# Optimization experiments

Measured on AMD Instinct MI355X. Metric: run time of the kernel, lower is better.

Reference implementation:

```python
import jax, jax.numpy as jnp
import numpy as np

N_VERTS = 778
N_JOINTS_CHAIN = 16  # wrist + 15 articulated joints
N_JOINTS_ALL = 21
PARENTS = np.array([0, 0, 1, 2, 0, 4, 5, 0, 7, 8, 0, 10, 11, 0, 13, 14])


def rodrigues(r):
    """Axis-angle [N,3] -> rotation matrices [N,3,3] (matches torch quat2mat path)."""
    angle = jnp.linalg.norm(r + 1e-8, axis=1, keepdims=True)  # [N,1]
    axis = r / angle
    c = jnp.cos(angle)[..., None]  # [N,1,1]
    s = jnp.sin(angle)[..., None]
    x, y, z = axis[:, 0], axis[:, 1], axis[:, 2]
    zero = jnp.zeros_like(x)
    K = jnp.stack([zero, -z, y,
                   z, zero, -x,
                   -y, x, zero], axis=1).reshape(-1, 3, 3)
    eye = jnp.eye(3, dtype=r.dtype)
    return eye + s * K + (1.0 - c) * jnp.matmul(K, K)


def make_A(R, t):
    """R [B,3,3], t [B,3] -> homogeneous [B,4,4]."""
    B = R.shape[0]
    top = jnp.concatenate([R, t[:, :, None]], axis=2)  # [B,3,4]
    bottom = jnp.broadcast_to(jnp.array([[[0., 0., 0., 1.]]], dtype=R.dtype), (B, 1, 4))
    return jnp.concatenate([top, bottom], axis=1)


def setup_inputs() -> dict:
    key = jax.random.key(0)
    ks = jax.random.split(key, 10)
    B = 8192
    w = jax.random.uniform(ks[9], (N_VERTS, 16), dtype=jnp.float32)
    w = w / jnp.sum(w, axis=1, keepdims=True)  # LBS weights rows sum to 1
    Jr = jax.random.uniform(ks[6], (N_VERTS, N_JOINTS_ALL), dtype=jnp.float32)
    Jr = Jr / jnp.sum(Jr, axis=0, keepdims=True)
    return {
        "beta": jax.random.normal(ks[0], (B, 10), dtype=jnp.float32) * 0.5,
        "theta": jax.random.normal(ks[1], (B, 10), dtype=jnp.float32) * 0.5,
        "wrist_euler": jax.random.normal(ks[2], (B, 3), dtype=jnp.float32) * 0.3,
        "v_template": jax.random.normal(ks[3], (N_VERTS, 3), dtype=jnp.float32) * 0.05,
        "shapedirs": jax.random.normal(ks[4], (10, N_VERTS * 3), dtype=jnp.float32) * 0.01,
        "posedirs": jax.random.normal(ks[5], (135, N_VERTS * 3), dtype=jnp.float32) * 0.01,
        "J_regressor": Jr,
        "hands_comp": jax.random.normal(ks[7], (10, 45), dtype=jnp.float32) * 0.5,
        "hands_mean": jax.random.normal(ks[8], (45,), dtype=jnp.float32) * 0.1,
        "weights": w,
    }


def reference(beta, theta, wrist_euler, v_template, shapedirs, posedirs,
              J_regressor, hands_comp, hands_mean, weights):
    B = beta.shape[0]
    # shape blendshapes
    v_shaped = jnp.matmul(beta, shapedirs).reshape(B, N_VERTS, 3) + v_template
    # joints from shaped template: [B,21,3]
    J = jnp.einsum('bvc,vj->bjc', v_shaped, J_regressor)
    # pca pose -> per-joint axis-angle -> rotation matrices
    euler_pose = jnp.matmul(theta, hands_comp) + hands_mean          # [B,45]
    Rs = rodrigues(euler_pose.reshape(-1, 3)).reshape(B, 15, 3, 3)
    global_rot = rodrigues(wrist_euler.reshape(-1, 3)).reshape(B, 1, 3, 3)
    # pose blendshapes: (Rs - I) flattened
    pose_feature = (Rs - jnp.eye(3, dtype=Rs.dtype)).reshape(B, 135)
    v_posed = v_shaped + jnp.matmul(pose_feature, posedirs).reshape(B, N_VERTS, 3)
    # kinematic chain (16 joints, fixed small loop)
    Rs_all = jnp.concatenate([global_rot, Rs], axis=1)  # [B,16,3,3]
    Jc = J[:, :N_JOINTS_CHAIN, :]
    results = [make_A(Rs_all[:, 0], Jc[:, 0])]
    for i in range(1, N_JOINTS_CHAIN):
        p = int(PARENTS[i])
        A_local = make_A(Rs_all[:, i], Jc[:, i] - Jc[:, p])
        results.append(jnp.matmul(results[p], A_local))
    G = jnp.stack(results, axis=1)  # [B,16,4,4]
    # subtract rest-pose joint locations: A = G - G @ [J;0] in last column
    Jh = jnp.concatenate([Jc, jnp.zeros((B, N_JOINTS_CHAIN, 1), Jc.dtype)], axis=2)
    GJ = jnp.einsum('bjpq,bjq->bjp', G, Jh)  # [B,16,4]
    A = G - jnp.concatenate([jnp.zeros((B, N_JOINTS_CHAIN, 4, 3), G.dtype), GJ[..., None]], axis=3)
    # linear blend skinning
    T = jnp.einsum('vj,bjpq->bvpq', weights, A)  # [B,778,4,4]
    v_posed_h = jnp.concatenate([v_posed, jnp.ones((B, N_VERTS, 1), v_posed.dtype)], axis=2)
    verts = jnp.einsum('bvpq,bvq->bvp', T, v_posed_h)[:, :, :3]
    joints = jnp.einsum('bvc,vj->bjc', verts, J_regressor)  # [B,21,3]
    return joints
```

## Files before the change

kernel.cpp:

```cpp
#include <hip/hip_runtime.h>
#include <math.h>

#define NV 778
#define KROW 2334
#define KTOT 146
#define NCOL 1008
#define NPART 16
#define DTLD 160
#define PEXLD 1032

__global__ __launch_bounds__(64) void kA_pre(const float* __restrict__ shapedirs,
                                             const float* __restrict__ posedirs,
                                             const float* __restrict__ v_template,
                                             const float* __restrict__ Jreg,
                                             const float* __restrict__ wgt,
                                             float* __restrict__ SJ, float* __restrict__ J0,
                                             float* __restrict__ Q,  float* __restrict__ W2,
                                             float* __restrict__ DT, int w2_blocks)
{
    const int bid = blockIdx.x;
    const int t = threadIdx.x;
    if (bid < 48) {
        const int j = bid / 3, c = bid % 3;
        float acc[11];
#pragma unroll
        for (int k = 0; k < 11; ++k) acc[k] = 0.f;
        for (int v = t; v < NV; v += 64) {
            const float jr = Jreg[v*21 + j];
            acc[10] += v_template[v*3 + c] * jr;
#pragma unroll
            for (int k = 0; k < 10; ++k)
                acc[k] += shapedirs[(size_t)k*KROW + v*3 + c] * jr;
        }
#pragma unroll
        for (int k = 0; k < 11; ++k) {
            float s = acc[k];
#pragma unroll
            for (int off = 32; off >= 1; off >>= 1) s += __shfl_down(s, off, 64);
            acc[k] = s;
        }
        if (t == 0) {
#pragma unroll
            for (int k = 0; k < 10; ++k) SJ[k*48 + j*3 + c] = acc[k];
            J0[j*3 + c] = acc[10];
        }
    } else if (bid < 384) {
        const int m = bid - 48, j = m >> 4, jj = m & 15;
        float s = 0.f;
        for (int v = t; v < NV; v += 64)
            s += Jreg[v*21 + j] * wgt[v*16 + jj];
#pragma unroll
        for (int off = 32; off >= 1; off >>= 1) s += __shfl_down(s, off, 64);
        if (t == 0) Q[m] = s;
    } else if (bid < 384 + w2_blocks) {
        const int gi = (bid - 384)*64 + t;
        if (gi < NV*336) {
            const int v = gi / 336, m = gi % 336;
            const int j = m >> 4, jj = m & 15;
            W2[gi] = Jreg[v*21 + j] * wgt[v*16 + jj];
        }
    } else {
        const int v = bid - 384 - w2_blocks;
#pragma unroll
        for (int kk = 0; kk < 3; ++kk) {
            const int k = t + kk*64;
            if (k < KTOT) {
                const float* drow = (k < 10)  ? shapedirs + (size_t)k*KROW
                                  : (k < 145) ? posedirs + (size_t)(k-10)*KROW
                                              : v_template;
                DT[((size_t)0*NV + v)*DTLD + k] = drow[3*v + 0];
                DT[((size_t)1*NV + v)*DTLD + k] = drow[3*v + 1];
                DT[((size_t)2*NV + v)*DTLD + k] = drow[3*v + 2];
            }
        }
    }
}

__global__ __launch_bounds__(192) void k_pre2(const float* __restrict__ DT,
                                              const float* __restrict__ W2,
                                              float* __restrict__ PKpart)
{
    const int bid = blockIdx.x;
    const int j = bid % 21;
    const int c = (bid / 21) % 3;
    const int s = bid / 63;
    const int k = threadIdx.x;
    if (k >= KTOT) return;
    float acc[16];
#pragma unroll
    for (int q = 0; q < 16; ++q) acc[q] = 0.f;
    const int v0 = s*49, v1 = min(NV, v0 + 49);
    const float* dt = DT + ((size_t)c*NV)*DTLD + k;
    for (int v = v0; v < v1; ++v) {
        const float d = dt[(size_t)v*DTLD];
        const float4* wq = (const float4*)(W2 + (size_t)v*336 + j*16);
        const float4 w0 = wq[0], w1 = wq[1], w2 = wq[2], w3 = wq[3];
        acc[0]  += d*w0.x; acc[1]  += d*w0.y; acc[2]  += d*w0.z; acc[3]  += d*w0.w;
        acc[4]  += d*w1.x; acc[5]  += d*w1.y; acc[6]  += d*w1.z; acc[7]  += d*w1.w;
        acc[8]  += d*w2.x; acc[9]  += d*w2.y; acc[10] += d*w2.z; acc[11] += d*w2.w;
        acc[12] += d*w3.x; acc[13] += d*w3.y; acc[14] += d*w3.z; acc[15] += d*w3.w;
    }
    float* o = PKpart + ((size_t)s*KTOT + k)*NCOL + j*48 + c;
#pragma unroll
    for (int q = 0; q < 16; ++q) o[q*3] = acc[q];
}

__global__ void k_p3(const float4* __restrict__ PKpart, float4* __restrict__ PK)
{
    const int n4 = KTOT*NCOL/4;
    const int idx = blockIdx.x*256 + threadIdx.x;
    if (idx < n4) {
        float4 s = PKpart[idx];
#pragma unroll
        for (int p = 1; p < NPART; ++p) {
            const float4 v = PKpart[(size_t)p*n4 + idx];
            s.x += v.x; s.y += v.y; s.z += v.z; s.w += v.w;
        }
        PK[idx] = s;
    }
}

__global__ __launch_bounds__(256) void k2_pose(const float* __restrict__ beta,
                                               const float* __restrict__ theta,
                                               const float* __restrict__ wrist,
                                               const float* __restrict__ hc,
                                               const float* __restrict__ hm,
                                               const float* __restrict__ SJ,
                                               const float* __restrict__ J0,
                                               float* __restrict__ coefT,
                                               float* __restrict__ A_g, int B)
{
    __shared__ float Rs[16*144];
    __shared__ float cls[16*148];
    const int t = threadIdx.x;
    const int bl = t >> 4, i = t & 15;
    const int b = blockIdx.x*16 + bl;

    float r0, r1, r2;
    if (i == 0) {
        r0 = wrist[b*3+0]; r1 = wrist[b*3+1]; r2 = wrist[b*3+2];
#pragma unroll
        for (int k = 0; k < 10; ++k) cls[bl*148 + k] = beta[b*10 + k];
        cls[bl*148 + 145] = 1.0f;
    } else {
        const int col = (i-1)*3;
        float e0 = hm[col], e1 = hm[col+1], e2 = hm[col+2];
#pragma unroll
        for (int k = 0; k < 10; ++k) {
            const float th = theta[b*10 + k];
            e0 += th * hc[k*45 + col];
            e1 += th * hc[k*45 + col+1];
            e2 += th * hc[k*45 + col+2];
        }
        r0 = e0; r1 = e1; r2 = e2;
    }
    const float x_ = r0 + 1e-8f, y_ = r1 + 1e-8f, z_ = r2 + 1e-8f;
    const float angle = sqrtf(x_*x_ + y_*y_ + z_*z_);
    const float inv = 1.0f / angle;
    const float x = r0*inv, y = r1*inv, z = r2*inv;
    const float sn = sinf(angle), cs = cosf(angle);
    const float t1 = 1.0f - cs;
    float R[9];
    R[0] = 1.f - t1*(y*y + z*z);
    R[1] = -sn*z + t1*x*y;
    R[2] =  sn*y + t1*x*z;
    R[3] =  sn*z + t1*x*y;
    R[4] = 1.f - t1*(x*x + z*z);
    R[5] = -sn*x + t1*y*z;
    R[6] = -sn*y + t1*x*z;
    R[7] =  sn*x + t1*y*z;
    R[8] = 1.f - t1*(x*x + y*y);
#pragma unroll
    for (int q = 0; q < 9; ++q) Rs[bl*144 + i*9 + q] = R[q];
    if (i > 0) {
#pragma unroll
        for (int q = 0; q < 9; ++q)
            cls[bl*148 + 10 + (i-1)*9 + q] = R[q] - ((q==0||q==4||q==8) ? 1.f : 0.f);
    }
    __syncthreads();

    if (t < KTOT) {
        float tmp[16];
#pragma unroll
        for (int m = 0; m < 16; ++m) tmp[m] = cls[m*148 + t];
        float4* dst = (float4*)(coefT + (size_t)t*B + blockIdx.x*16);
        dst[0] = make_float4(tmp[0],  tmp[1],  tmp[2],  tmp[3]);
        dst[1] = make_float4(tmp[4],  tmp[5],  tmp[6],  tmp[7]);
        dst[2] = make_float4(tmp[8],  tmp[9],  tmp[10], tmp[11]);
        dst[3] = make_float4(tmp[12], tmp[13], tmp[14], tmp[15]);
    }

    if (t < 16) {
        const int b2 = blockIdx.x*16 + t;
        float bt[10];
#pragma unroll
        for (int k = 0; k < 10; ++k) bt[k] = beta[b2*10 + k];
        const float* Rb = Rs + t*144;
        float4* Ab = (float4*)(A_g + (size_t)b2*192);

        auto jointJ = [&](int j, float* o) {
            float j0 = J0[j*3+0], j1 = J0[j*3+1], j2 = J0[j*3+2];
#pragma unroll
            for (int k = 0; k < 10; ++k) {
                j0 += bt[k] * SJ[k*48 + j*3 + 0];
                j1 += bt[k] * SJ[k*48 + j*3 + 1];
                j2 += bt[k] * SJ[k*48 + j*3 + 2];
            }
            o[0] = j0; o[1] = j1; o[2] = j2;
        };

        float G0R[9], J0v[3];
#pragma unroll
        for (int q = 0; q < 9; ++q) G0R[q] = Rb[q];
        jointJ(0, J0v);
#pragma unroll
        for (int r = 0; r < 3; ++r) {
            const float at = J0v[r] - (G0R[r*3+0]*J0v[0] + G0R[r*3+1]*J0v[1] + G0R[r*3+2]*J0v[2]);
            Ab[r] = make_float4(G0R[r*3+0], G0R[r*3+1], G0R[r*3+2], at);
        }
        for (int ch = 0; ch < 5; ++ch) {
            float GpR[9], Gpt[3], Jp[3];
#pragma unroll
            for (int q = 0; q < 9; ++q) GpR[q] = G0R[q];
            Gpt[0]=J0v[0]; Gpt[1]=J0v[1]; Gpt[2]=J0v[2];
            Jp[0]=J0v[0];  Jp[1]=J0v[1];  Jp[2]=J0v[2];
            for (int s = 0; s < 3; ++s) {
                const int j = ch*3 + 1 + s;
                float Rl[9];
                const float* Rj = Rb + j*9;
#pragma unroll
                for (int q = 0; q < 9; ++q) Rl[q] = Rj[q];
                float Jc[3];
                jointJ(j, Jc);
                const float tl0 = Jc[0]-Jp[0], tl1 = Jc[1]-Jp[1], tl2 = Jc[2]-Jp[2];
                float GR[9], Gt[3];
#pragma unroll
                for (int r = 0; r < 3; ++r) {
#pragma unroll
                    for (int cc = 0; cc < 3; ++cc)
                        GR[r*3+cc] = GpR[r*3+0]*Rl[0*3+cc] + GpR[r*3+1]*Rl[1*3+cc] + GpR[r*3+2]*Rl[2*3+cc];
                    Gt[r] = GpR[r*3+0]*tl0 + GpR[r*3+1]*tl1 + GpR[r*3+2]*tl2 + Gpt[r];
                }
#pragma unroll
                for (int r = 0; r < 3; ++r) {
                    const float at = Gt[r] - (GR[r*3+0]*Jc[0] + GR[r*3+1]*Jc[1] + GR[r*3+2]*Jc[2]);
                    Ab[j*3 + r] = make_float4(GR[r*3+0], GR[r*3+1], GR[r*3+2], at);
                }
#pragma unroll
                for (int q = 0; q < 9; ++q) GpR[q] = GR[q];
                Gpt[0]=Gt[0]; Gpt[1]=Gt[1]; Gpt[2]=Gt[2];
                Jp[0]=Jc[0];  Jp[1]=Jc[1];  Jp[2]=Jc[2];
            }
        }
    }
}

__global__ __launch_bounds__(512) void k3_gemm(const float* __restrict__ coefT,
                                               const float* __restrict__ PK,
                                               const float* __restrict__ A_g,
                                               const float* __restrict__ Q,
                                               float* __restrict__ out, int B)
{
    __shared__ float Pex[8*PEXLD];
    const int t  = threadIdx.x;
    const int b0 = blockIdx.x * 16;
    const int l  = t;

    float acc[2][16];
#pragma unroll
    for (int e = 0; e < 16; ++e) { acc[0][e] = 0.f; acc[1][e] = 0.f; }

    if (l < 504) {
        const float* pkp = PK + 2*l;
        const float* cof = coefT + b0;
#pragma unroll 2
        for (int k = 0; k < KTOT; ++k) {
            const float2 p2 = *(const float2*)(pkp + (size_t)k*NCOL);
            const float4* cp = (const float4*)(cof + (size_t)k*B);
            const float4 c0 = cp[0], c1 = cp[1], c2 = cp[2], c3 = cp[3];
            const float cv[16] = {c0.x,c0.y,c0.z,c0.w, c1.x,c1.y,c1.z,c1.w,
                                  c2.x,c2.y,c2.z,c2.w, c3.x,c3.y,c3.z,c3.w};
#pragma unroll
            for (int e = 0; e < 16; ++e) {
                acc[0][e] += p2.x * cv[e];
                acc[1][e] += p2.y * cv[e];
            }
        }
    }

#pragma unroll
    for (int r = 0; r < 2; ++r) {
        __syncthreads();
        if (l < 504) {
            const int j  = (2*l) / 48;
            const int sc = j*49 + (2*l - 48*j);
#pragma unroll
            for (int bb = 0; bb < 8; ++bb)
                *(float2*)(&Pex[bb*PEXLD + sc]) =
                    make_float2(acc[0][r*8 + bb], acc[1][r*8 + bb]);
        }
        __syncthreads();
        if (t < 504) {
            const int bl = t / 63;
            const int rm = t % 63;
            const int j  = rm / 3, p = rm % 3;
            const int b  = b0 + r*8 + bl;
            const float4* Ab = ((const float4*)A_g) + (size_t)b*48;
            const float* Pr = Pex + bl*PEXLD + j*49;
            float s = 0.f;
#pragma unroll
            for (int jj = 0; jj < 16; ++jj) {
                const float4 a = Ab[jj*3 + p];
                s += a.x*Pr[jj*3+0] + a.y*Pr[jj*3+1] + a.z*Pr[jj*3+2]
                   + a.w*Q[j*16+jj];
            }
            out[(size_t)b0*63 + r*504 + t] = s;
        }
    }
}

extern "C" void kernel_launch(void* const* d_in, const int* in_sizes, int n_in,
                              void* d_out, int out_size, void* d_ws, size_t ws_size,
                              hipStream_t stream) {
    (void)n_in; (void)out_size; (void)ws_size;
    const float* beta       = (const float*)d_in[0];
    const float* theta      = (const float*)d_in[1];
    const float* wrist      = (const float*)d_in[2];
    const float* v_template = (const float*)d_in[3];
    const float* shapedirs  = (const float*)d_in[4];
    const float* posedirs   = (const float*)d_in[5];
    const float* Jreg       = (const float*)d_in[6];
    const float* hc         = (const float*)d_in[7];
    const float* hm         = (const float*)d_in[8];
    const float* wgt        = (const float*)d_in[9];
    float* out = (float*)d_out;
    const int B = in_sizes[0] / 10;

    float* ws = (float*)d_ws;
    size_t off = 0;
    auto alloc = [&](size_t n) { float* p = ws + off; off = (off + n + 63) & ~(size_t)63; return p; };
    float* SJ     = alloc(480);
    float* J0     = alloc(48);
    float* Q      = alloc(336);
    float* W2     = alloc((size_t)NV*336);
    float* DT     = alloc((size_t)3*NV*DTLD);
    float* PKpart = alloc((size_t)NPART*KTOT*NCOL);
    float* PK     = alloc((size_t)KTOT*NCOL);
    float* coefT  = alloc((size_t)KTOT*B);
    float* A_g    = alloc((size_t)B*192);

    const int w2_blocks = (NV*336 + 63)/64;
    kA_pre<<<384 + w2_blocks + NV, 64, 0, stream>>>(shapedirs, posedirs, v_template,
                                                    Jreg, wgt, SJ, J0, Q, W2, DT, w2_blocks);
    k2_pose<<<(B + 15)/16, 256, 0, stream>>>(beta, theta, wrist, hc, hm, SJ, J0, coefT, A_g, B);
    k_pre2<<<21*3*NPART, 192, 0, stream>>>(DT, W2, PKpart);
    k_p3<<<(KTOT*NCOL/4 + 255)/256, 256, 0, stream>>>((const float4*)PKpart, (float4*)PK);
    k3_gemm<<<dim3(B/16), 512, 0, stream>>>(coefT, PK, A_g, Q, out, B);
}
```

Before: 164.2 us.

## Merge precompute kernels and replace partial-sum reduction with atomics

The parameter precompute stages are cut from four launches to two. The PK partial-product kernel now runs inside the same launch as the pose kernel and adds its results straight into PK with atomicAdd, so the PKpart buffer and its separate reduction kernel are gone. The first kernel zeroes PK and moves to 256-thread blocks, with one wave per reduction row. Vertex splitting doubles to 32 parts so there are more parallel blocks, at the cost of many more float atomics and a summation order that is no longer deterministic.

```diff
diff --git a/kernel.cpp b/kernel.cpp
--- a/kernel.cpp
+++ b/kernel.cpp
@@ -5,27 +5,36 @@
 #define KROW 2334
 #define KTOT 146
 #define NCOL 1008
-#define NPART 16
+#define NPART 32
 #define DTLD 160
 #define PEXLD 1032
 
-__global__ __launch_bounds__(64) void kA_pre(const float* __restrict__ shapedirs,
-                                             const float* __restrict__ posedirs,
-                                             const float* __restrict__ v_template,
-                                             const float* __restrict__ Jreg,
-                                             const float* __restrict__ wgt,
-                                             float* __restrict__ SJ, float* __restrict__ J0,
-                                             float* __restrict__ Q,  float* __restrict__ W2,
-                                             float* __restrict__ DT, int w2_blocks)
+#define NB_RED 12
+#define NB_Q   84
+#define NB_W2  ((NV*336 + 255)/256)
+#define NB_DT  NV
+#define NB_Z   ((KTOT*NCOL + 255)/256)
+
+__global__ __launch_bounds__(256) void kA_all(const float* __restrict__ shapedirs,
+                                              const float* __restrict__ posedirs,
+                                              const float* __restrict__ v_template,
+                                              const float* __restrict__ Jreg,
+                                              const float* __restrict__ wgt,
+                                              float* __restrict__ SJ, float* __restrict__ J0,
+                                              float* __restrict__ Q,  float* __restrict__ W2,
+                                              float* __restrict__ DT, float* __restrict__ PK)
 {
     const int bid = blockIdx.x;
     const int t = threadIdx.x;
-    if (bid < 48) {
-        const int j = bid / 3, c = bid % 3;
+    const int wv = t >> 6, lane = t & 63;
+
+    if (bid < NB_RED) {
+        const int m = bid*4 + wv;
+        const int j = m / 3, c = m % 3;
         float acc[11];
 #pragma unroll
         for (int k = 0; k < 11; ++k) acc[k] = 0.f;
-        for (int v = t; v < NV; v += 64) {
+        for (int v = lane; v < NV; v += 64) {
             const float jr = Jreg[v*21 + j];
             acc[10] += v_template[v*3 + c] * jr;
 #pragma unroll
@@ -39,102 +48,91 @@
             for (int off = 32; off >= 1; off >>= 1) s += __shfl_down(s, off, 64);
             acc[k] = s;
         }
-        if (t == 0) {
+        if (lane == 0) {
 #pragma unroll
             for (int k = 0; k < 10; ++k) SJ[k*48 + j*3 + c] = acc[k];
             J0[j*3 + c] = acc[10];
         }
-    } else if (bid < 384) {
-        const int m = bid - 48, j = m >> 4, jj = m & 15;
+    } else if (bid < NB_RED + NB_Q) {
+        const int m = (bid - NB_RED)*4 + wv;
+        const int j = m >> 4, jj = m & 15;
         float s = 0.f;
-        for (int v = t; v < NV; v += 64)
+        for (int v = lane; v < NV; v += 64)
             s += Jreg[v*21 + j] * wgt[v*16 + jj];
 #pragma unroll
         for (int off = 32; off >= 1; off >>= 1) s += __shfl_down(s, off, 64);
-        if (t == 0) Q[m] = s;
-    } else if (bid < 384 + w2_blocks) {
-        const int gi = (bid - 384)*64 + t;
+        if (lane == 0) Q[m] = s;
+    } else if (bid < NB_RED + NB_Q + NB_W2) {
+        const int gi = (bid - NB_RED - NB_Q)*256 + t;
         if (gi < NV*336) {
             const int v = gi / 336, m = gi % 336;
             const int j = m >> 4, jj = m & 15;
             W2[gi] = Jreg[v*21 + j] * wgt[v*16 + jj];
         }
+    } else if (bid < NB_RED + NB_Q + NB_W2 + NB_DT) {
+        const int v = bid - NB_RED - NB_Q - NB_W2;
+        const int k = t;
+        if (k < KTOT) {
+            const float* drow = (k < 10)  ? shapedirs + (size_t)k*KROW
+                              : (k < 145) ? posedirs + (size_t)(k-10)*KROW
+                                          : v_template;
+            DT[((size_t)0*NV + v)*DTLD + k] = drow[3*v + 0];
+            DT[((size_t)1*NV + v)*DTLD + k] = drow[3*v + 1];
+            DT[((size_t)2*NV + v)*DTLD + k] = drow[3*v + 2];
+        }
     } else {
-        const int v = bid - 384 - w2_blocks;
-#pragma unroll
-        for (int kk = 0; kk < 3; ++kk) {
-            const int k = t + kk*64;
-            if (k < KTOT) {
-                const float* drow = (k < 10)  ? shapedirs + (size_t)k*KROW
-                                  : (k < 145) ? posedirs + (size_t)(k-10)*KROW
-                                              : v_template;
-                DT[((size_t)0*NV + v)*DTLD + k] = drow[3*v + 0];
-                DT[((size_t)1*NV + v)*DTLD + k] = drow[3*v + 1];
-                DT[((size_t)2*NV + v)*DTLD + k] = drow[3*v + 2];
-            }
-        }
+        const int idx = (bid - NB_RED - NB_Q - NB_W2 - NB_DT)*256 + t;
+        if (idx < KTOT*NCOL) PK[idx] = 0.f;
     }
 }
 
-__global__ __launch_bounds__(192) void k_pre2(const float* __restrict__ DT,
-                                              const float* __restrict__ W2,
-                                              float* __restrict__ PKpart)
-{
-    const int bid = blockIdx.x;
-    const int j = bid % 21;
-    const int c = (bid / 21) % 3;
-    const int s = bid / 63;
-    const int k = threadIdx.x;
-    if (k >= KTOT) return;
-    float acc[16];
-#pragma unroll
-    for (int q = 0; q < 16; ++q) acc[q] = 0.f;
-    const int v0 = s*49, v1 = min(NV, v0 + 49);
-    const float* dt = DT + ((size_t)c*NV)*DTLD + k;
-    for (int v = v0; v < v1; ++v) {
-        const float d = dt[(size_t)v*DTLD];
-        const float4* wq = (const float4*)(W2 + (size_t)v*336 + j*16);
-        const float4 w0 = wq[0], w1 = wq[1], w2 = wq[2], w3 = wq[3];
-        acc[0]  += d*w0.x; acc[1]  += d*w0.y; acc[2]  += d*w0.z; acc[3]  += d*w0.w;
-        acc[4]  += d*w1.x; acc[5]  += d*w1.y; acc[6]  += d*w1.z; acc[7]  += d*w1.w;
-        acc[8]  += d*w2.x; acc[9]  += d*w2.y; acc[10] += d*w2.z; acc[11] += d*w2.w;
-        acc[12] += d*w3.x; acc[13] += d*w3.y; acc[14] += d*w3.z; acc[15] += d*w3.w;
-    }
-    float* o = PKpart + ((size_t)s*KTOT + k)*NCOL + j*48 + c;
-#pragma unroll
-    for (int q = 0; q < 16; ++q) o[q*3] = acc[q];
-}
-
-__global__ void k_p3(const float4* __restrict__ PKpart, float4* __restrict__ PK)
-{
-    const int n4 = KTOT*NCOL/4;
-    const int idx = blockIdx.x*256 + threadIdx.x;
-    if (idx < n4) {
-        float4 s = PKpart[idx];
-#pragma unroll
-        for (int p = 1; p < NPART; ++p) {
-            const float4 v = PKpart[(size_t)p*n4 + idx];
-            s.x += v.x; s.y += v.y; s.z += v.z; s.w += v.w;
-        }
-        PK[idx] = s;
-    }
-}
-
-__global__ __launch_bounds__(256) void k2_pose(const float* __restrict__ beta,
-                                               const float* __restrict__ theta,
-                                               const float* __restrict__ wrist,
-                                               const float* __restrict__ hc,
-                                               const float* __restrict__ hm,
-                                               const float* __restrict__ SJ,
-                                               const float* __restrict__ J0,
-                                               float* __restrict__ coefT,
-                                               float* __restrict__ A_g, int B)
+__global__ __launch_bounds__(256) void k_mid(const float* __restrict__ DT,
+                                             const float* __restrict__ W2,
+                                             float* __restrict__ PK,
+                                             const float* __restrict__ beta,
+                                             const float* __restrict__ theta,
+                                             const float* __restrict__ wrist,
+                                             const float* __restrict__ hc,
+                                             const float* __restrict__ hm,
+                                             const float* __restrict__ SJ,
+                                             const float* __restrict__ J0,
+                                             float* __restrict__ coefT,
+                                             float* __restrict__ A_g, int B)
 {
     __shared__ float Rs[16*144];
     __shared__ float cls[16*148];
+    const int bid = blockIdx.x;
     const int t = threadIdx.x;
+
+    if (bid < 21*3*NPART) {
+        const int j = bid % 21;
+        const int c = (bid / 21) % 3;
+        const int s = bid / 63;
+        const int k = t;
+        if (k >= KTOT) return;
+        float acc[16];
+#pragma unroll
+        for (int q = 0; q < 16; ++q) acc[q] = 0.f;
+        const int v0 = s*25, v1 = min(NV, v0 + 25);
+        const float* dt = DT + ((size_t)c*NV)*DTLD + k;
+        for (int v = v0; v < v1; ++v) {
+            const float d = dt[(size_t)v*DTLD];
+            const float4* wq = (const float4*)(W2 + (size_t)v*336 + j*16);
+            const float4 w0 = wq[0], w1 = wq[1], w2 = wq[2], w3 = wq[3];
+            acc[0]  += d*w0.x; acc[1]  += d*w0.y; acc[2]  += d*w0.z; acc[3]  += d*w0.w;
+            acc[4]  += d*w1.x; acc[5]  += d*w1.y; acc[6]  += d*w1.z; acc[7]  += d*w1.w;
+            acc[8]  += d*w2.x; acc[9]  += d*w2.y; acc[10] += d*w2.z; acc[11] += d*w2.w;
+            acc[12] += d*w3.x; acc[13] += d*w3.y; acc[14] += d*w3.z; acc[15] += d*w3.w;
+        }
+        float* o = PK + (size_t)k*NCOL + j*48 + c;
+#pragma unroll
+        for (int q = 0; q < 16; ++q) atomicAdd(o + q*3, acc[q]);
+        return;
+    }
+
+    const int kb = bid - 21*3*NPART;
     const int bl = t >> 4, i = t & 15;
-    const int b = blockIdx.x*16 + bl;
+    const int b = kb*16 + bl;
 
     float r0, r1, r2;
     if (i == 0) {
@@ -183,7 +181,7 @@
         float tmp[16];
 #pragma unroll
         for (int m = 0; m < 16; ++m) tmp[m] = cls[m*148 + t];
-        float4* dst = (float4*)(coefT + (size_t)t*B + blockIdx.x*16);
+        float4* dst = (float4*)(coefT + (size_t)t*B + kb*16);
         dst[0] = make_float4(tmp[0],  tmp[1],  tmp[2],  tmp[3]);
         dst[1] = make_float4(tmp[4],  tmp[5],  tmp[6],  tmp[7]);
         dst[2] = make_float4(tmp[8],  tmp[9],  tmp[10], tmp[11]);
@@ -191,7 +189,7 @@
     }
 
     if (t < 16) {
-        const int b2 = blockIdx.x*16 + t;
+        const int b2 = kb*16 + t;
         float bt[10];
 #pragma unroll
         for (int k = 0; k < 10; ++k) bt[k] = beta[b2*10 + k];
@@ -344,16 +342,16 @@
     float* Q      = alloc(336);
     float* W2     = alloc((size_t)NV*336);
     float* DT     = alloc((size_t)3*NV*DTLD);
-    float* PKpart = alloc((size_t)NPART*KTOT*NCOL);
     float* PK     = alloc((size_t)KTOT*NCOL);
     float* coefT  = alloc((size_t)KTOT*B);
     float* A_g    = alloc((size_t)B*192);
 
-    const int w2_blocks = (NV*336 + 63)/64;
-    kA_pre<<<384 + w2_blocks + NV, 64, 0, stream>>>(shapedirs, posedirs, v_template,
-                                                    Jreg, wgt, SJ, J0, Q, W2, DT, w2_blocks);
-    k2_pose<<<(B + 15)/16, 256, 0, stream>>>(beta, theta, wrist, hc, hm, SJ, J0, coefT, A_g, B);
-    k_pre2<<<21*3*NPART, 192, 0, stream>>>(DT, W2, PKpart);
-    k_p3<<<(KTOT*NCOL/4 + 255)/256, 256, 0, stream>>>((const float4*)PKpart, (float4*)PK);
+    const int nb1 = NB_RED + NB_Q + NB_W2 + NB_DT + NB_Z;
+    const int nb2 = 21*3*NPART + (B + 15)/16;
+
+    kA_all<<<nb1, 256, 0, stream>>>(shapedirs, posedirs, v_template, Jreg, wgt,
+                                    SJ, J0, Q, W2, DT, PK);
+    k_mid<<<nb2, 256, 0, stream>>>(DT, W2, PK, beta, theta, wrist, hc, hm,
+                                   SJ, J0, coefT, A_g, B);
     k3_gemm<<<dim3(B/16), 512, 0, stream>>>(coefT, PK, A_g, Q, out, B);
 }
```

Result: slower. 377.4 us (+129.9%).
